# Optimization experiments

Measured on AMD Instinct MI355X. Metric: run time of the kernel, lower is better.

Reference implementation:

```python
import jax, jax.numpy as jnp
import numpy as np

N_SEGMENT = 8  # frames per clip
N_DIV = 8      # fold divisor: fold = C // N_DIV channels shift each way


def setup_inputs() -> dict:
    key = jax.random.key(0)
    k1, k2 = jax.random.split(key)
    x = jax.random.normal(k1, (128, 256, 28, 28), dtype=jnp.float32)  # [nt, C, H, W], nt = 16 clips * 8 frames
    net_weight = jax.random.normal(k2, (256, 256), dtype=jnp.float32) * 0.0625  # 1x1 conv [out_c, in_c]
    return {"x": x, "net_weight": net_weight}


def temporal_shift(x):
    # x: [nt, C, H, W]. Equivalent to the fixed one-hot depthwise Conv3d (k=3, pad=1):
    #   channels [:fold]        -> out[t] = x[t-1]  (weight[...,0]=1)
    #   channels [fold:2*fold]  -> out[t] = x[t+1]  (weight[...,2]=1)
    #   channels [2*fold:]      -> out[t] = x[t]    (weight[...,1]=1)
    nt, c, h, w = x.shape
    b = nt // N_SEGMENT
    xv = x.reshape(b, N_SEGMENT, c, h, w)
    fold = c // N_DIV
    prev = jnp.pad(xv[:, :-1, :fold], ((0, 0), (1, 0), (0, 0), (0, 0), (0, 0)))       # shift right in time
    nxt = jnp.pad(xv[:, 1:, fold:2 * fold], ((0, 0), (0, 1), (0, 0), (0, 0), (0, 0)))  # shift left in time
    shifted = jnp.concatenate([prev, nxt, xv[:, :, 2 * fold:]], axis=2)
    return shifted.reshape(nt, c, h, w)


def reference(x, net_weight):
    y = temporal_shift(x)
    # wrapped net: 1x1 Conv2d(256 -> 256, bias=False) == per-pixel GEMM
    out = jnp.einsum('nchw,oc->nohw', y, net_weight)
    return out
```

## Files before the change

### kernel.cpp

```cpp
#include <hip/hip_runtime.h>
#include <hip/hip_bf16.h>


#define CDIM 256
#define HWPX 784
#define FRST (CDIM * HWPX)
#define P_TILE 112
#define NPT  7
#define NWG  (128 * NPT * 2)
#define LROW 264

using bf16x8 = __attribute__((ext_vector_type(8))) short;
using f32x4  = __attribute__((ext_vector_type(4))) float;

static __device__ __forceinline__ unsigned int pk2(float lo, float hi) {
    union { __hip_bfloat162 h; unsigned int u; } cv;
    cv.h = __float22bfloat162_rn(make_float2(lo, hi));
    return cv.u;
}

__global__ void wconv(const float* __restrict__ w, unsigned short* __restrict__ wb) {
    const int i = (blockIdx.x * 256 + threadIdx.x) * 4;
    f32x4 v = *(const f32x4*)(w + i);
    *(uint2*)(wb + i) = make_uint2(pk2(v[0], v[1]), pk2(v[2], v[3]));
}

__global__ __launch_bounds__(256, 2)
void tsm_deep(const float* __restrict__ x,
              const unsigned short* __restrict__ wb,
              float* __restrict__ out) {
    __shared__ __align__(16) unsigned short y[P_TILE * LROW];

    const int bid = blockIdx.x;
    const int wg  = (bid & 7) * (NWG / 8) + (bid >> 3);
    const int h    = wg & 1;
    const int pair = wg >> 1;
    const int n    = pair / NPT;
    const int pt   = pair - n * NPT;
    const int p0   = pt * P_TILE;
    const int tid  = threadIdx.x;
    const int tf   = n & 7;

    const int lane = tid & 63;
    const int wv   = tid >> 6;
    const int g    = lane >> 4;
    const int ol   = lane & 15;

    bf16x8 wf[8][2];
    #pragma unroll
    for (int kk = 0; kk < 8; ++kk)
        #pragma unroll
        for (int m = 0; m < 2; ++m) {
            const unsigned short* wp =
                &wb[(size_t)(h * 128 + wv * 32 + m * 16 + ol) * CDIM + kk * 32 + g * 8];
            asm volatile("global_load_dwordx4 %0, %1, off"
                         : "=v"(wf[kk][m]) : "v"(wp));
        }

    f32x4 r0[14], r1[14];
    #pragma unroll
    for (int i = 0; i < 14; ++i) {
        const int idx = tid + i * 256;
        const int cp  = idx / 28;
        const int pv  = idx - cp * 28;
        const int c0  = cp * 2;
        const int d   = (cp < 16) ? -1 : (cp < 32 ? 1 : 0);
        const bool valid = !((d == -1 && tf == 0) || (d == 1 && tf == 7));
        const float* s = x + ((size_t)(n + (valid ? d : 0)) * CDIM + c0) * HWPX
                           + p0 + pv * 4;
        asm volatile("global_load_dwordx4 %0, %1, off" : "=v"(r0[i]) : "v"(s));
        const float* s1 = s + HWPX;
        asm volatile("global_load_dwordx4 %0, %1, off" : "=v"(r1[i]) : "v"(s1));
    }
    asm volatile("s_waitcnt vmcnt(0)" ::: "memory");
    __builtin_amdgcn_sched_barrier(0);

    #pragma unroll
    for (int i = 0; i < 14; ++i) {
        const int idx = tid + i * 256;
        const int cp  = idx / 28;
        const int pv  = idx - cp * 28;
        const int c0  = cp * 2;
        const int d   = (cp < 16) ? -1 : (cp < 32 ? 1 : 0);
        const bool valid = !((d == -1 && tf == 0) || (d == 1 && tf == 7));
        const int cc = c0 ^ ((pv & 7) << 3);
        const int rb = pv * 4 * LROW + cc;
        #pragma unroll
        for (int r = 0; r < 4; ++r)
            *(unsigned int*)&y[rb + r * LROW] =
                valid ? pk2(r0[i][r], r1[i][r]) : 0u;
    }
    __syncthreads();

    f32x4 acc[2][7];
    #pragma unroll
    for (int m = 0; m < 2; ++m)
        #pragma unroll
        for (int nn = 0; nn < 7; ++nn)
            acc[m][nn] = f32x4{0.f, 0.f, 0.f, 0.f};

    #pragma unroll
    for (int kk = 0; kk < 8; ++kk) {
        const int c = kk * 32 + g * 8;
        #pragma unroll
        for (int nn = 0; nn < 7; ++nn) {
            const int p  = nn * 16 + ol;
            const int cc = c ^ (((p >> 2) & 7) << 3);
            const bf16x8 bf = *(const bf16x8*)&y[p * LROW + cc];
            acc[0][nn] = __builtin_amdgcn_mfma_f32_16x16x32_bf16(wf[kk][0], bf, acc[0][nn], 0, 0, 0);
            acc[1][nn] = __builtin_amdgcn_mfma_f32_16x16x32_bf16(wf[kk][1], bf, acc[1][nn], 0, 0, 0);
        }
    }

    const size_t outbase = (size_t)n * CDIM * HWPX + p0 + ol;
    #pragma unroll
    for (int m = 0; m < 2; ++m) {
        #pragma unroll
        for (int r = 0; r < 4; ++r) {
            const int o = h * 128 + wv * 32 + m * 16 + g * 4 + r;
            float* orow = out + outbase + (size_t)o * HWPX;
            #pragma unroll
            for (int nn = 0; nn < 7; ++nn)
                orow[nn * 16] = acc[m][nn][r];
        }
    }
}

#define LDS_STRIDE 264
__global__ __launch_bounds__(512, 4)
void tsm_fallback(const float* __restrict__ x, const float* __restrict__ w,
                  float* __restrict__ out) {
    __shared__ __align__(16) unsigned short ylds[P_TILE * LDS_STRIDE];
    const int n = blockIdx.x, tile = blockIdx.y, p0 = tile * P_TILE;
    const int tid = threadIdx.x, tf = n & 7;
    f32x4 v0[7], v1[7]; int cps[7], pvs[7];
    #pragma unroll
    for (int i = 0; i < 7; ++i) {
        const int idx = tid + i * 512, cp = idx / 28, pv = idx - cp * 28;
        cps[i] = cp; pvs[i] = pv;
        const int c0 = cp * 2;
        int nsrc; bool valid;
        if (c0 < 32)      { nsrc = n - 1; valid = (tf > 0); }
        else if (c0 < 64) { nsrc = n + 1; valid = (tf < 7); }
        else              { nsrc = n;     valid = true; }
        const float* src = x + ((size_t)(valid ? nsrc : n) * CDIM + c0) * HWPX + p0 + pv * 4;
        f32x4 a = {0,0,0,0}, b = {0,0,0,0};
        if (valid) { a = *(const f32x4*)src; b = *(const f32x4*)(src + HWPX); }
        v0[i] = a; v1[i] = b;
    }
    #pragma unroll
    for (int i = 0; i < 7; ++i) {
        const int c0 = cps[i] * 2, pv = pvs[i];
        const int cc = c0 ^ ((pv & 7) << 3);
        const int rb = pv * 4 * LDS_STRIDE + cc;
        #pragma unroll
        for (int r = 0; r < 4; ++r)
            *(unsigned int*)&ylds[rb + r * LDS_STRIDE] = pk2(v0[i][r], v1[i][r]);
    }
    __syncthreads();
    const int lane = tid & 63, wv = tid >> 6, g = lane >> 4, ol = lane & 15;
    f32x4 acc[2][7];
    #pragma unroll
    for (int m = 0; m < 2; ++m)
        #pragma unroll
        for (int nn = 0; nn < 7; ++nn) acc[m][nn] = f32x4{0,0,0,0};
    #pragma unroll
    for (int kk = 0; kk < 8; ++kk) {
        const int c = kk * 32 + g * 8;
        bf16x8 af[2];
        #pragma unroll
        for (int m = 0; m < 2; ++m) {
            const float* wp = w + (size_t)(wv * 32 + m * 16 + ol) * CDIM + c;
            f32x4 w0 = *(const f32x4*)wp, w1 = *(const f32x4*)(wp + 4);
            union { bf16x8 v; unsigned int u4[4]; } cv;
            cv.u4[0] = pk2(w0[0], w0[1]); cv.u4[1] = pk2(w0[2], w0[3]);
            cv.u4[2] = pk2(w1[0], w1[1]); cv.u4[3] = pk2(w1[2], w1[3]);
            af[m] = cv.v;
        }
        #pragma unroll
        for (int nn = 0; nn < 7; ++nn) {
            const int p = nn * 16 + ol;
            const int cc = c ^ (((p >> 2) & 7) << 3);
            const bf16x8 bf = *(const bf16x8*)&ylds[p * LDS_STRIDE + cc];
            #pragma unroll
            for (int m = 0; m < 2; ++m)
                acc[m][nn] = __builtin_amdgcn_mfma_f32_16x16x32_bf16(af[m], bf, acc[m][nn], 0, 0, 0);
        }
    }
    const size_t outbase = (size_t)n * CDIM * HWPX + p0 + ol;
    #pragma unroll
    for (int m = 0; m < 2; ++m)
        #pragma unroll
        for (int r = 0; r < 4; ++r) {
            const int o = wv * 32 + m * 16 + g * 4 + r;
            float* orow = out + outbase + (size_t)o * HWPX;
            #pragma unroll
            for (int nn = 0; nn < 7; ++nn) orow[nn * 16] = acc[m][nn][r];
        }
}

extern "C" void kernel_launch(void* const* d_in, const int* in_sizes, int n_in,
                              void* d_out, int out_size, void* d_ws, size_t ws_size,
                              hipStream_t stream) {
    const float* x = (const float*)d_in[0];
    const float* w = (const float*)d_in[1];
    float* out     = (float*)d_out;
    const size_t wb_bytes = (size_t)CDIM * CDIM * sizeof(unsigned short);
    if (ws_size >= wb_bytes) {
        unsigned short* wbuf = (unsigned short*)d_ws;
        wconv<<<64, 256, 0, stream>>>(w, wbuf);
        tsm_deep<<<NWG, 256, 0, stream>>>(x, wbuf, out);
    } else {
        tsm_fallback<<<dim3(128, 7, 1), dim3(512, 1, 1), 0, stream>>>(x, w, out);
    }
}
```

Before: 50.44 us.

## Split LDS staging in two halves to overlap second-half loads with MFMA

The kernel now waits only for the first half of the activation loads (channels 0-127) and stages them into shared memory. It runs the MFMA loop over the first four K-steps while the remaining loads are still in flight, then stages the second half and finishes the K loop. The LDS swizzle is changed to XOR 4-element groups, and each 8-element operand is read as two 4-element loads. This adds a second barrier and more LDS read instructions in exchange for hiding part of the global-load latency.

```diff
diff --git a/kernel.cpp b/kernel.cpp
--- a/kernel.cpp
+++ b/kernel.cpp
@@ -11,6 +11,7 @@
 #define LROW 264
 
 using bf16x8 = __attribute__((ext_vector_type(8))) short;
+using bf16x4 = __attribute__((ext_vector_type(4))) short;
 using f32x4  = __attribute__((ext_vector_type(4))) float;
 
 static __device__ __forceinline__ unsigned int pk2(float lo, float hi) {
@@ -26,9 +27,9 @@
 }
 
 __global__ __launch_bounds__(256, 2)
-void tsm_deep(const float* __restrict__ x,
-              const unsigned short* __restrict__ wb,
-              float* __restrict__ out) {
+void tsm_ksplit(const float* __restrict__ x,
+                const unsigned short* __restrict__ wb,
+                float* __restrict__ out) {
     __shared__ __align__(16) unsigned short y[P_TILE * LROW];
 
     const int bid = blockIdx.x;
@@ -72,45 +73,68 @@
         const float* s1 = s + HWPX;
         asm volatile("global_load_dwordx4 %0, %1, off" : "=v"(r1[i]) : "v"(s1));
     }
+
+    #define WRITE_ITEM(i)                                                      \
+    {                                                                          \
+        const int idx = tid + (i) * 256;                                       \
+        const int cp  = idx / 28;                                              \
+        const int pv  = idx - cp * 28;                                         \
+        const int c0  = cp * 2;                                                \
+        const int d   = (cp < 16) ? -1 : (cp < 32 ? 1 : 0);                    \
+        const bool valid = !((d == -1 && tf == 0) || (d == 1 && tf == 7));     \
+        const int cc  = c0 ^ (((pv >> 1) & 7) << 2);       \
+        const int rb  = pv * 4 * LROW + cc;                                    \
+        _Pragma("unroll")                                                      \
+        for (int r = 0; r < 4; ++r)                                            \
+            *(unsigned int*)&y[rb + r * LROW] =                                \
+                valid ? pk2(r0[i][r], r1[i][r]) : 0u;                          \
+    }
+
+    asm volatile("s_waitcnt vmcnt(14)" ::: "memory");
+    __builtin_amdgcn_sched_barrier(0);
+    #pragma unroll
+    for (int i = 0; i < 7; ++i) WRITE_ITEM(i)
+    __syncthreads();
+
+    f32x4 acc[2][7];
+    #pragma unroll
+    for (int m = 0; m < 2; ++m)
+        #pragma unroll
+        for (int nn = 0; nn < 7; ++nn)
+            acc[m][nn] = f32x4{0.f, 0.f, 0.f, 0.f};
+
+    #define COMPUTE(K0, K1)                                                    \
+    {                                                                          \
+        _Pragma("unroll")                                                      \
+        for (int nn = 0; nn < 7; ++nn) {                                       \
+            const int p    = nn * 16 + ol;                                     \
+            const int zz   = ((p >> 3) & 7) << 2;                              \
+            const int rowb = p * LROW;                                         \
+            _Pragma("unroll")                                                  \
+            for (int kk = (K0); kk < (K1); ++kk) {                             \
+                const int c  = kk * 32 + g * 8;                                \
+                const int e0 = c ^ zz;                                         \
+                const bf16x4 lo = *(const bf16x4*)&y[rowb + e0];               \
+                const bf16x4 hi = *(const bf16x4*)&y[rowb + (e0 ^ 4)];         \
+                const bf16x8 bf = __builtin_shufflevector(lo, hi,              \
+                                                          0, 1, 2, 3, 4, 5, 6, 7); \
+                acc[0][nn] = __builtin_amdgcn_mfma_f32_16x16x32_bf16(          \
+                    wf[kk][0], bf, acc[0][nn], 0, 0, 0);                       \
+                acc[1][nn] = __builtin_amdgcn_mfma_f32_16x16x32_bf16(          \
+                    wf[kk][1], bf, acc[1][nn], 0, 0, 0);                       \
+            }                                                                  \
+        }                                                                      \
+    }
+
+    COMPUTE(0, 4)
+
     asm volatile("s_waitcnt vmcnt(0)" ::: "memory");
     __builtin_amdgcn_sched_barrier(0);
-
-    #pragma unroll
-    for (int i = 0; i < 14; ++i) {
-        const int idx = tid + i * 256;
-        const int cp  = idx / 28;
-        const int pv  = idx - cp * 28;
-        const int c0  = cp * 2;
-        const int d   = (cp < 16) ? -1 : (cp < 32 ? 1 : 0);
-        const bool valid = !((d == -1 && tf == 0) || (d == 1 && tf == 7));
-        const int cc = c0 ^ ((pv & 7) << 3);
-        const int rb = pv * 4 * LROW + cc;
-        #pragma unroll
-        for (int r = 0; r < 4; ++r)
-            *(unsigned int*)&y[rb + r * LROW] =
-                valid ? pk2(r0[i][r], r1[i][r]) : 0u;
-    }
+    #pragma unroll
+    for (int i = 7; i < 14; ++i) WRITE_ITEM(i)
     __syncthreads();
 
-    f32x4 acc[2][7];
-    #pragma unroll
-    for (int m = 0; m < 2; ++m)
-        #pragma unroll
-        for (int nn = 0; nn < 7; ++nn)
-            acc[m][nn] = f32x4{0.f, 0.f, 0.f, 0.f};
-
-    #pragma unroll
-    for (int kk = 0; kk < 8; ++kk) {
-        const int c = kk * 32 + g * 8;
-        #pragma unroll
-        for (int nn = 0; nn < 7; ++nn) {
-            const int p  = nn * 16 + ol;
-            const int cc = c ^ (((p >> 2) & 7) << 3);
-            const bf16x8 bf = *(const bf16x8*)&y[p * LROW + cc];
-            acc[0][nn] = __builtin_amdgcn_mfma_f32_16x16x32_bf16(wf[kk][0], bf, acc[0][nn], 0, 0, 0);
-            acc[1][nn] = __builtin_amdgcn_mfma_f32_16x16x32_bf16(wf[kk][1], bf, acc[1][nn], 0, 0, 0);
-        }
-    }
+    COMPUTE(4, 8)
 
     const size_t outbase = (size_t)n * CDIM * HWPX + p0 + ol;
     #pragma unroll
@@ -124,6 +148,8 @@
                 orow[nn * 16] = acc[m][nn][r];
         }
     }
+    #undef WRITE_ITEM
+    #undef COMPUTE
 }
 
 #define LDS_STRIDE 264
@@ -209,7 +235,7 @@
     if (ws_size >= wb_bytes) {
         unsigned short* wbuf = (unsigned short*)d_ws;
         wconv<<<64, 256, 0, stream>>>(w, wbuf);
-        tsm_deep<<<NWG, 256, 0, stream>>>(x, wbuf, out);
+        tsm_ksplit<<<NWG, 256, 0, stream>>>(x, wbuf, out);
     } else {
         tsm_fallback<<<dim3(128, 7, 1), dim3(512, 1, 1), 0, stream>>>(x, w, out);
     }
```

Result: faster. 48.59 us, median of 3 (-3.7%).
